# Optimization experiments

Hardware: AMD Instinct MI355X
Metric: run time of the kernel (lower is better)

The kernel has to match this reference:

```python
import jax, jax.numpy as jnp
import numpy as np

EPS = 1e-06
SIGMA_C = 2.0


def setup_inputs() -> dict:
    key = jax.random.key(0)
    k1, k2 = jax.random.split(key)
    B, L, D, T = 16, 512, 256, 2048
    text = jax.random.normal(k1, (B, L, D), dtype=jnp.float32)
    durs = jax.random.randint(k2, (B, L), 0, 8, dtype=jnp.int64)
    return {"text": text, "durs": durs, "total_time": T}


def reference(text, durs, total_time):
    # text: [B, L, D], durs: [B, L] int, total_time: static python int T
    d = durs.astype(jnp.float32)
    # NOTE: faithful to original: mean = durs/2 + cumsum(durs) (cumsum includes current dur)
    mean = d / 2.0 + jnp.cumsum(d, axis=-1)            # [B, L]
    sigma = d / SIGMA_C + EPS                          # [B, L]
    t = jnp.arange(total_time, dtype=jnp.float32) + 0.5  # [T]
    # Normal pdf evaluated at t: exp(log_prob) = exp(-0.5 z^2) / (sigma * sqrt(2 pi))
    z = (t[None, :, None] - mean[:, None, :]) / sigma[:, None, :]  # [B, T, L]
    inv_norm = 1.0 / (sigma[:, None, :] * jnp.sqrt(2.0 * jnp.pi))
    probs = jnp.exp(-0.5 * z * z) * inv_norm           # [B, T, L]
    probs = probs / (probs.sum(-1, keepdims=True) + EPS)
    return jnp.einsum("btl,bld->btd", probs, text)     # [B, T, D]
```

## Files before the change

### kernel.cpp

```cpp
#include <hip/hip_runtime.h>
#include <math.h>

#define L 512
#define TILE_T 16
#define NTHREADS 256
#define NACT_MAX 160
#define ZWIN 14.5f
#define NXCD 8

static constexpr float EPS = 1e-6f;
static constexpr float INV_SQRT_2PI = 0.39894228040143267794f;

__global__ __launch_bounds__(NTHREADS, 8) void ge_kernel(
    const float* __restrict__ text,
    const int*   __restrict__ durs,
    float*       __restrict__ out,
    int B, int D, int T, int tilesPerB, int nwg)
{
    __shared__ float s_lmean[NACT_MAX];
    __shared__ float s_lisig[NACT_MAX];
    __shared__ int   s_lrow[NACT_MAX];
    __shared__ float s_probs[NACT_MAX][TILE_T];
    __shared__ float s_wtot[4];
    __shared__ int   s_wcnt[4];
    __shared__ float s_wsum[4][TILE_T];
    __shared__ float s_norm[TILE_T];

    const int tid  = threadIdx.x;
    const int lane = tid & 63;
    const int wid  = tid >> 6;

    const int orig = blockIdx.x;
    const int wg   = (orig & (NXCD - 1)) * (nwg / NXCD) + (orig >> 3);
    const int b    = wg / tilesPerB;
    const int t0   = (wg % tilesPerB) * TILE_T;

    const int l0 = 2 * tid;
    const float d0 = (float)durs[b * L + l0];
    const float d1 = (float)durs[b * L + l0 + 1];
    const float pairsum = d0 + d1;

    float v = pairsum;
    #pragma unroll
    for (int off = 1; off < 64; off <<= 1) {
        float n = __shfl_up(v, off, 64);
        if (lane >= off) v += n;
    }
    if (lane == 63) s_wtot[wid] = v;
    __syncthreads();
    float wpre = 0.f;
    for (int w = 0; w < wid; ++w) wpre += s_wtot[w];
    const float excl = wpre + v - pairsum;

    const float cum0  = excl + d0;
    const float cum1  = cum0 + d1;
    const float mean0 = cum0 + 0.5f * d0;
    const float mean1 = cum1 + 0.5f * d1;
    const float sig0  = 0.5f * d0 + EPS;
    const float sig1  = 0.5f * d1 + EPS;
    const float isig0 = 1.0f / sig0;
    const float isig1 = 1.0f / sig1;

    const float tlo = (float)t0 + 0.5f;
    const float thi = (float)t0 + (float)TILE_T - 0.5f;
    const float r0 = ZWIN * sig0;
    const float r1 = ZWIN * sig1;
    const bool act0 = (d0 >= 1.f) && (mean0 + r0 >= tlo) && (mean0 - r0 <= thi);
    const bool act1 = (d1 >= 1.f) && (mean1 + r1 >= tlo) && (mean1 - r1 <= thi);

    const unsigned long long m0 = __ballot(act0);
    const unsigned long long m1 = __ballot(act1);
    const unsigned long long lt = (lane == 0) ? 0ull : ((~0ull) >> (64 - lane));
    const int off_in_wave = __popcll(m0 & lt) + __popcll(m1 & lt);
    const int cnt_wave = __popcll(m0) + __popcll(m1);
    if (lane == 0) s_wcnt[wid] = cnt_wave;
    __syncthreads();
    int base_w = 0;
    for (int w = 0; w < wid; ++w) base_w += s_wcnt[w];
    const int nact = s_wcnt[0] + s_wcnt[1] + s_wcnt[2] + s_wcnt[3];

    if (act0) {
        const int i = base_w + off_in_wave;
        s_lrow[i] = l0; s_lmean[i] = mean0; s_lisig[i] = isig0;
    }
    if (act1) {
        const int i = base_w + off_in_wave + (act0 ? 1 : 0);
        s_lrow[i] = l0 + 1; s_lmean[i] = mean1; s_lisig[i] = isig1;
    }
    __syncthreads();

    float psum = 0.f;
    const int   mytt = tid & 15;
    const float myt  = (float)(t0 + mytt) + 0.5f;
    const int total = nact * TILE_T;
    for (int idx = tid; idx < total; idx += NTHREADS) {
        const int i = idx >> 4;
        const float isg = s_lisig[i];
        const float z = (myt - s_lmean[i]) * isg;
        const float p = __expf(-0.5f * z * z) * isg * INV_SQRT_2PI;
        s_probs[i][mytt] = p;
        psum += p;
    }
    psum += __shfl_xor(psum, 16, 64);
    psum += __shfl_xor(psum, 32, 64);
    if (lane < 16) s_wsum[wid][lane] = psum;
    __syncthreads();
    if (tid < TILE_T) {
        const float s = s_wsum[0][tid] + s_wsum[1][tid] + s_wsum[2][tid] + s_wsum[3][tid];
        s_norm[tid] = 1.0f / (s + EPS);
    }
    __syncthreads();

    float4 a0 = {0,0,0,0}, a1 = {0,0,0,0}, a2 = {0,0,0,0}, a3 = {0,0,0,0};
    const float* tbase = text + (size_t)b * L * D + (lane << 2);
    if (nact > 0) {
        float4 vnext = *(const float4*)(tbase + (size_t)s_lrow[0] * D);
        for (int i = 0; i < nact; ++i) {
            const float4 val = vnext;
            if (i + 1 < nact)
                vnext = *(const float4*)(tbase + (size_t)s_lrow[i + 1] * D);
            const float4 p = *(const float4*)&s_probs[i][wid << 2];
            a0.x += p.x * val.x; a0.y += p.x * val.y; a0.z += p.x * val.z; a0.w += p.x * val.w;
            a1.x += p.y * val.x; a1.y += p.y * val.y; a1.z += p.y * val.z; a1.w += p.y * val.w;
            a2.x += p.z * val.x; a2.y += p.z * val.y; a2.z += p.z * val.z; a2.w += p.z * val.w;
            a3.x += p.w * val.x; a3.y += p.w * val.y; a3.z += p.w * val.z; a3.w += p.w * val.w;
        }
    }

    const float4 nrm = *(const float4*)&s_norm[wid << 2];
    const int tt0 = t0 + (wid << 2);
    float* obase = out + ((size_t)b * T + tt0) * D + (lane << 2);
    { float4 o = {a0.x*nrm.x, a0.y*nrm.x, a0.z*nrm.x, a0.w*nrm.x}; *(float4*)(obase + 0*(size_t)D) = o; }
    { float4 o = {a1.x*nrm.y, a1.y*nrm.y, a1.z*nrm.y, a1.w*nrm.y}; *(float4*)(obase + 1*(size_t)D) = o; }
    { float4 o = {a2.x*nrm.z, a2.y*nrm.z, a2.z*nrm.z, a2.w*nrm.z}; *(float4*)(obase + 2*(size_t)D) = o; }
    { float4 o = {a3.x*nrm.w, a3.y*nrm.w, a3.z*nrm.w, a3.w*nrm.w}; *(float4*)(obase + 3*(size_t)D) = o; }
}

extern "C" void kernel_launch(void* const* d_in, const int* in_sizes, int n_in,
                              void* d_out, int out_size, void* d_ws, size_t ws_size,
                              hipStream_t stream) {
    const float* text = (const float*)d_in[0];
    const int*   durs = (const int*)d_in[1];
    float*       out  = (float*)d_out;

    const int BL = in_sizes[1];
    const int D  = in_sizes[0] / BL;
    const int B  = BL / L;
    const int T  = out_size / (B * D);
    const int tilesPerB = (T + TILE_T - 1) / TILE_T;
    const int nwg = B * tilesPerB;

    ge_kernel<<<dim3(nwg), dim3(NTHREADS), 0, stream>>>(
        text, durs, out, B, D, T, tilesPerB, nwg);
}
```

Measured before the change: 18.09 us.

## Make each wave independently compute scan, active list, probs and norms without block barriers

Each wave now redundantly computes the full prefix sum over durations using int4 loads and an intra-wave scan. It then builds its own compacted active list for its 4 time steps and computes probabilities and normalisers with wave shuffles, which removes all __syncthreads. The Gaussian window shrinks from 14.5 to 9 sigma, the list is padded so the text-row gather loop can be unrolled by two, and bounds checks are added on the stores. The trade-off is redundant scan work per wave and a narrower truncation window, which may change numerics slightly.

New measurement: 19.05 us. 1.05x slower.

```diff
diff --git a/kernel.cpp b/kernel.cpp
--- a/kernel.cpp
+++ b/kernel.cpp
@@ -4,8 +4,9 @@
 #define L 512
 #define TILE_T 16
 #define NTHREADS 256
-#define NACT_MAX 160
-#define ZWIN 14.5f
+#define NWAVES 4
+#define NACT_PAD 104
+#define ZWIN 9.0f
 #define NXCD 8
 
 static constexpr float EPS = 1e-6f;
@@ -17,14 +18,9 @@
     float*       __restrict__ out,
     int B, int D, int T, int tilesPerB, int nwg)
 {
-    __shared__ float s_lmean[NACT_MAX];
-    __shared__ float s_lisig[NACT_MAX];
-    __shared__ int   s_lrow[NACT_MAX];
-    __shared__ float s_probs[NACT_MAX][TILE_T];
-    __shared__ float s_wtot[4];
-    __shared__ int   s_wcnt[4];
-    __shared__ float s_wsum[4][TILE_T];
-    __shared__ float s_norm[TILE_T];
+    __shared__ float2 s_mi [NWAVES][NACT_PAD];
+    __shared__ int    s_row[NWAVES][NACT_PAD];
+    __shared__ float  s_p  [NWAVES][4][NACT_PAD];
 
     const int tid  = threadIdx.x;
     const int lane = tid & 63;
@@ -35,105 +31,130 @@
     const int b    = wg / tilesPerB;
     const int t0   = (wg % tilesPerB) * TILE_T;
 
-    const int l0 = 2 * tid;
-    const float d0 = (float)durs[b * L + l0];
-    const float d1 = (float)durs[b * L + l0 + 1];
-    const float pairsum = d0 + d1;
-
-    float v = pairsum;
-    #pragma unroll
-    for (int off = 1; off < 64; off <<= 1) {
-        float n = __shfl_up(v, off, 64);
-        if (lane >= off) v += n;
+    const int r0 = lane << 3;
+    const int4* dp = (const int4*)(durs + (size_t)b * L + r0);
+    const int4 da = dp[0];
+    const int4 db = dp[1];
+    int dv[8] = {da.x, da.y, da.z, da.w, db.x, db.y, db.z, db.w};
+    int csum[8];
+    {
+        int run = 0;
+        #pragma unroll
+        for (int j = 0; j < 8; ++j) { run += dv[j]; csum[j] = run; }
+        int v = run;
+        #pragma unroll
+        for (int off = 1; off < 64; off <<= 1) {
+            int n = __shfl_up(v, off, 64);
+            if (lane >= off) v += n;
+        }
+        const int excl = v - run;
+        #pragma unroll
+        for (int j = 0; j < 8; ++j) csum[j] += excl;
     }
-    if (lane == 63) s_wtot[wid] = v;
-    __syncthreads();
-    float wpre = 0.f;
-    for (int w = 0; w < wid; ++w) wpre += s_wtot[w];
-    const float excl = wpre + v - pairsum;
-
-    const float cum0  = excl + d0;
-    const float cum1  = cum0 + d1;
-    const float mean0 = cum0 + 0.5f * d0;
-    const float mean1 = cum1 + 0.5f * d1;
-    const float sig0  = 0.5f * d0 + EPS;
-    const float sig1  = 0.5f * d1 + EPS;
-    const float isig0 = 1.0f / sig0;
-    const float isig1 = 1.0f / sig1;
 
     const float tlo = (float)t0 + 0.5f;
     const float thi = (float)t0 + (float)TILE_T - 0.5f;
-    const float r0 = ZWIN * sig0;
-    const float r1 = ZWIN * sig1;
-    const bool act0 = (d0 >= 1.f) && (mean0 + r0 >= tlo) && (mean0 - r0 <= thi);
-    const bool act1 = (d1 >= 1.f) && (mean1 + r1 >= tlo) && (mean1 - r1 <= thi);
 
-    const unsigned long long m0 = __ballot(act0);
-    const unsigned long long m1 = __ballot(act1);
-    const unsigned long long lt = (lane == 0) ? 0ull : ((~0ull) >> (64 - lane));
-    const int off_in_wave = __popcll(m0 & lt) + __popcll(m1 & lt);
-    const int cnt_wave = __popcll(m0) + __popcll(m1);
-    if (lane == 0) s_wcnt[wid] = cnt_wave;
-    __syncthreads();
-    int base_w = 0;
-    for (int w = 0; w < wid; ++w) base_w += s_wcnt[w];
-    const int nact = s_wcnt[0] + s_wcnt[1] + s_wcnt[2] + s_wcnt[3];
+    float meanv[8], isigv[8];
+    bool  act[8];
+    #pragma unroll
+    for (int j = 0; j < 8; ++j) {
+        const float d  = (float)dv[j];
+        const float m  = (float)csum[j] + 0.5f * d;
+        const float sg = 0.5f * d + EPS;
+        meanv[j] = m;
+        isigv[j] = 1.0f / sg;
+        const float r = ZWIN * sg;
+        act[j] = (dv[j] >= 1) && (m + r >= tlo) && (m - r <= thi);
+    }
+    const unsigned long long ltm = (lane == 0) ? 0ull : ((~0ull) >> (64 - lane));
+    int nact = 0;
+    #pragma unroll
+    for (int j = 0; j < 8; ++j) {
+        const unsigned long long mj = __ballot(act[j]);
+        if (act[j]) {
+            const int idx = nact + (int)__popcll(mj & ltm);
+            s_mi [wid][idx] = make_float2(meanv[j], isigv[j]);
+            s_row[wid][idx] = r0 + j;
+        }
+        nact += (int)__popcll(mj);
+    }
+    if (lane < 4) {
+        s_row[wid][nact + lane]  = 0;
+        s_p[wid][0][nact + lane] = 0.f;
+        s_p[wid][1][nact + lane] = 0.f;
+        s_p[wid][2][nact + lane] = 0.f;
+        s_p[wid][3][nact + lane] = 0.f;
+    }
+    asm volatile("s_waitcnt lgkmcnt(0)" ::: "memory");
+    __builtin_amdgcn_sched_barrier(0);
 
-    if (act0) {
-        const int i = base_w + off_in_wave;
-        s_lrow[i] = l0; s_lmean[i] = mean0; s_lisig[i] = isig0;
+    const float tq = (float)(t0 + (wid << 2)) + 0.5f;
+    float ps0 = 0.f, ps1 = 0.f, ps2 = 0.f, ps3 = 0.f;
+    for (int base_i = 0; base_i < nact; base_i += 64) {
+        const int item = base_i + lane;
+        if (item < nact) {
+            const float2 mi = s_mi[wid][item];
+            const float c  = mi.y * INV_SQRT_2PI;
+            const float z0 = (tq + 0.f - mi.x) * mi.y;
+            const float z1 = (tq + 1.f - mi.x) * mi.y;
+            const float z2 = (tq + 2.f - mi.x) * mi.y;
+            const float z3 = (tq + 3.f - mi.x) * mi.y;
+            const float p0 = __expf(-0.5f * z0 * z0) * c;
+            const float p1 = __expf(-0.5f * z1 * z1) * c;
+            const float p2 = __expf(-0.5f * z2 * z2) * c;
+            const float p3 = __expf(-0.5f * z3 * z3) * c;
+            s_p[wid][0][item] = p0;
+            s_p[wid][1][item] = p1;
+            s_p[wid][2][item] = p2;
+            s_p[wid][3][item] = p3;
+            ps0 += p0; ps1 += p1; ps2 += p2; ps3 += p3;
+        }
     }
-    if (act1) {
-        const int i = base_w + off_in_wave + (act0 ? 1 : 0);
-        s_lrow[i] = l0 + 1; s_lmean[i] = mean1; s_lisig[i] = isig1;
+    #pragma unroll
+    for (int off = 32; off > 0; off >>= 1) {
+        ps0 += __shfl_xor(ps0, off, 64);
+        ps1 += __shfl_xor(ps1, off, 64);
+        ps2 += __shfl_xor(ps2, off, 64);
+        ps3 += __shfl_xor(ps3, off, 64);
     }
-    __syncthreads();
-
-    float psum = 0.f;
-    const int   mytt = tid & 15;
-    const float myt  = (float)(t0 + mytt) + 0.5f;
-    const int total = nact * TILE_T;
-    for (int idx = tid; idx < total; idx += NTHREADS) {
-        const int i = idx >> 4;
-        const float isg = s_lisig[i];
-        const float z = (myt - s_lmean[i]) * isg;
-        const float p = __expf(-0.5f * z * z) * isg * INV_SQRT_2PI;
-        s_probs[i][mytt] = p;
-        psum += p;
-    }
-    psum += __shfl_xor(psum, 16, 64);
-    psum += __shfl_xor(psum, 32, 64);
-    if (lane < 16) s_wsum[wid][lane] = psum;
-    __syncthreads();
-    if (tid < TILE_T) {
-        const float s = s_wsum[0][tid] + s_wsum[1][tid] + s_wsum[2][tid] + s_wsum[3][tid];
-        s_norm[tid] = 1.0f / (s + EPS);
-    }
-    __syncthreads();
+    const float rn0 = 1.0f / (ps0 + EPS);
+    const float rn1 = 1.0f / (ps1 + EPS);
+    const float rn2 = 1.0f / (ps2 + EPS);
+    const float rn3 = 1.0f / (ps3 + EPS);
+    asm volatile("s_waitcnt lgkmcnt(0)" ::: "memory");
+    __builtin_amdgcn_sched_barrier(0);
 
     float4 a0 = {0,0,0,0}, a1 = {0,0,0,0}, a2 = {0,0,0,0}, a3 = {0,0,0,0};
-    const float* tbase = text + (size_t)b * L * D + (lane << 2);
+    const float* tb = text + (size_t)b * L * D + (lane << 2);
     if (nact > 0) {
-        float4 vnext = *(const float4*)(tbase + (size_t)s_lrow[0] * D);
-        for (int i = 0; i < nact; ++i) {
-            const float4 val = vnext;
-            if (i + 1 < nact)
-                vnext = *(const float4*)(tbase + (size_t)s_lrow[i + 1] * D);
-            const float4 p = *(const float4*)&s_probs[i][wid << 2];
-            a0.x += p.x * val.x; a0.y += p.x * val.y; a0.z += p.x * val.z; a0.w += p.x * val.w;
-            a1.x += p.y * val.x; a1.y += p.y * val.y; a1.z += p.y * val.z; a1.w += p.y * val.w;
-            a2.x += p.z * val.x; a2.y += p.z * val.y; a2.z += p.z * val.z; a2.w += p.z * val.w;
-            a3.x += p.w * val.x; a3.y += p.w * val.y; a3.z += p.w * val.z; a3.w += p.w * val.w;
+        float4 v0 = *(const float4*)(tb + (size_t)s_row[wid][0] * D);
+        float4 v1 = *(const float4*)(tb + (size_t)s_row[wid][1] * D);
+        const int niter = (nact + 1) & ~1;
+        for (int i = 0; i < niter; i += 2) {
+            const float4 w0 = v0;
+            const float4 w1 = v1;
+            v0 = *(const float4*)(tb + (size_t)s_row[wid][i + 2] * D);
+            v1 = *(const float4*)(tb + (size_t)s_row[wid][i + 3] * D);
+            const float q00 = s_p[wid][0][i],     q10 = s_p[wid][1][i],     q20 = s_p[wid][2][i],     q30 = s_p[wid][3][i];
+            const float q01 = s_p[wid][0][i + 1], q11 = s_p[wid][1][i + 1], q21 = s_p[wid][2][i + 1], q31 = s_p[wid][3][i + 1];
+            a0.x += q00*w0.x; a0.y += q00*w0.y; a0.z += q00*w0.z; a0.w += q00*w0.w;
+            a1.x += q10*w0.x; a1.y += q10*w0.y; a1.z += q10*w0.z; a1.w += q10*w0.w;
+            a2.x += q20*w0.x; a2.y += q20*w0.y; a2.z += q20*w0.z; a2.w += q20*w0.w;
+            a3.x += q30*w0.x; a3.y += q30*w0.y; a3.z += q30*w0.z; a3.w += q30*w0.w;
+            a0.x += q01*w1.x; a0.y += q01*w1.y; a0.z += q01*w1.z; a0.w += q01*w1.w;
+            a1.x += q11*w1.x; a1.y += q11*w1.y; a1.z += q11*w1.z; a1.w += q11*w1.w;
+            a2.x += q21*w1.x; a2.y += q21*w1.y; a2.z += q21*w1.z; a2.w += q21*w1.w;
+            a3.x += q31*w1.x; a3.y += q31*w1.y; a3.z += q31*w1.z; a3.w += q31*w1.w;
         }
     }
 
-    const float4 nrm = *(const float4*)&s_norm[wid << 2];
-    const int tt0 = t0 + (wid << 2);
-    float* obase = out + ((size_t)b * T + tt0) * D + (lane << 2);
-    { float4 o = {a0.x*nrm.x, a0.y*nrm.x, a0.z*nrm.x, a0.w*nrm.x}; *(float4*)(obase + 0*(size_t)D) = o; }
-    { float4 o = {a1.x*nrm.y, a1.y*nrm.y, a1.z*nrm.y, a1.w*nrm.y}; *(float4*)(obase + 1*(size_t)D) = o; }
-    { float4 o = {a2.x*nrm.z, a2.y*nrm.z, a2.z*nrm.z, a2.w*nrm.z}; *(float4*)(obase + 2*(size_t)D) = o; }
-    { float4 o = {a3.x*nrm.w, a3.y*nrm.w, a3.z*nrm.w, a3.w*nrm.w}; *(float4*)(obase + 3*(size_t)D) = o; }
+    const int ttq = t0 + (wid << 2);
+    float* ob = out + ((size_t)b * T + ttq) * D + (lane << 2);
+    if (ttq + 0 < T) *(float4*)(ob + 0*(size_t)D) = make_float4(a0.x*rn0, a0.y*rn0, a0.z*rn0, a0.w*rn0);
+    if (ttq + 1 < T) *(float4*)(ob + 1*(size_t)D) = make_float4(a1.x*rn1, a1.y*rn1, a1.z*rn1, a1.w*rn1);
+    if (ttq + 2 < T) *(float4*)(ob + 2*(size_t)D) = make_float4(a2.x*rn2, a2.y*rn2, a2.z*rn2, a2.w*rn2);
+    if (ttq + 3 < T) *(float4*)(ob + 3*(size_t)D) = make_float4(a3.x*rn3, a3.y*rn3, a3.z*rn3, a3.w*rn3);
 }
 
 extern "C" void kernel_launch(void* const* d_in, const int* in_sizes, int n_in,
```

## Use bf16 MFMA with pre-transposed text and contiguous active window

Applied to the files above, without the earlier changes.

Adds a prep kernel that transposes text to a padded bf16 [B,D,L] workspace, then a main kernel that computes the Gaussian weights in registers as bf16 A fragments and accumulates with 16x16x32 bf16 MFMA over a contiguous range of active L indices. It narrows the z-window and drops the LDS probs staging, compaction and several block barriers. The intent is to replace scalar FP32 FMA loops and gather-style text loads with matrix-core work. In exchange it adds an extra launch plus a full text read/write each call, and bf16 rounding of weights and text, which lowers accuracy. The old kernel stays as a fallback when D differs or the workspace is too small.

New measurement: 21.32 us. +17.9%, slower.

```diff
diff --git a/kernel.cpp b/kernel.cpp
--- a/kernel.cpp
+++ b/kernel.cpp
@@ -4,18 +4,160 @@
 #define L 512
 #define TILE_T 16
 #define NTHREADS 256
-#define NACT_MAX 160
-#define ZWIN 14.5f
+#define ZWIN 9.0f
 #define NXCD 8
+#define LPAD 544
+
+typedef __attribute__((ext_vector_type(8))) short bf16x8;
+typedef __attribute__((ext_vector_type(4))) float f32x4;
 
 static constexpr float EPS = 1e-6f;
 static constexpr float INV_SQRT_2PI = 0.39894228040143267794f;
 
-__global__ __launch_bounds__(NTHREADS, 8) void ge_kernel(
-    const float* __restrict__ text,
-    const int*   __restrict__ durs,
-    float*       __restrict__ out,
-    int B, int D, int T, int tilesPerB, int nwg)
+__device__ __forceinline__ unsigned int rne_bf16(float f) {
+    const unsigned int u = __float_as_uint(f);
+    return (u + 0x7fffu + ((u >> 16) & 1u)) >> 16;
+}
+
+__global__ __launch_bounds__(NTHREADS) void ge_prep(
+    const float* __restrict__ text, unsigned short* __restrict__ tT)
+{
+    const int tid = threadIdx.x;
+    const int b   = blockIdx.x >> 4;
+    const int l0  = (blockIdx.x & 15) << 5;
+    const float* src = text + ((size_t)b * L + l0) * 256 + tid;
+    unsigned int pk[16];
+    #pragma unroll
+    for (int j = 0; j < 16; ++j) {
+        const float f0 = src[(size_t)(2 * j) * 256];
+        const float f1 = src[(size_t)(2 * j + 1) * 256];
+        pk[j] = rne_bf16(f0) | (rne_bf16(f1) << 16);
+    }
+    uint4* dst = (uint4*)(tT + ((size_t)b * 256 + tid) * LPAD + l0);
+    dst[0] = make_uint4(pk[0],  pk[1],  pk[2],  pk[3]);
+    dst[1] = make_uint4(pk[4],  pk[5],  pk[6],  pk[7]);
+    dst[2] = make_uint4(pk[8],  pk[9],  pk[10], pk[11]);
+    dst[3] = make_uint4(pk[12], pk[13], pk[14], pk[15]);
+}
+
+__global__ __launch_bounds__(NTHREADS, 6) void ge_mfma(
+    const int*            __restrict__ durs,
+    const unsigned short* __restrict__ tT,
+    float*                __restrict__ out,
+    int B, int T, int tilesPerB, int nwg)
+{
+    __shared__ float2 s_mi[L];
+    __shared__ float  s_rn[TILE_T];
+
+    const int tid  = threadIdx.x;
+    const int lane = tid & 63;
+    const int wid  = tid >> 6;
+    const int g    = lane >> 4;
+    const int mrow = lane & 15;
+
+    const int orig = blockIdx.x;
+    const int wg   = (nwg % NXCD == 0) ? (orig & (NXCD - 1)) * (nwg / NXCD) + (orig >> 3)
+                                       : orig;
+    const int b    = wg / tilesPerB;
+    const int t0   = (wg % tilesPerB) * TILE_T;
+
+    const int r0 = lane << 3;
+    const int4 da = ((const int4*)(durs + (size_t)b * L + r0))[0];
+    const int4 db = ((const int4*)(durs + (size_t)b * L + r0))[1];
+    int dv[8] = {da.x, da.y, da.z, da.w, db.x, db.y, db.z, db.w};
+    int cs[8];
+    int run = 0;
+    #pragma unroll
+    for (int j = 0; j < 8; ++j) { run += dv[j]; cs[j] = run; }
+    int v = run;
+    #pragma unroll
+    for (int off = 1; off < 64; off <<= 1) {
+        int n = __shfl_up(v, off, 64);
+        if (lane >= off) v += n;
+    }
+    const int excl = v - run;
+
+    const float tlo = (float)t0 + 0.5f, thi = (float)t0 + 15.5f;
+    int mn = L, mx = -1;
+    #pragma unroll
+    for (int j = 0; j < 8; ++j) {
+        const float d  = (float)dv[j];
+        const float m  = (float)(cs[j] + excl) + 0.5f * d;
+        const float sg = 0.5f * d + EPS;
+        s_mi[r0 + j] = make_float2(m, 1.0f / sg);
+        const float r = ZWIN * sg;
+        if (dv[j] >= 1 && m + r >= tlo && m - r <= thi) {
+            mn = min(mn, r0 + j);
+            mx = max(mx, r0 + j);
+        }
+    }
+    #pragma unroll
+    for (int off = 32; off > 0; off >>= 1) {
+        mn = min(mn, __shfl_xor(mn, off, 64));
+        mx = max(mx, __shfl_xor(mx, off, 64));
+    }
+    asm volatile("s_waitcnt lgkmcnt(0)" ::: "memory");
+    __builtin_amdgcn_sched_barrier(0);
+
+    f32x4 acc0 = {0,0,0,0}, acc1 = {0,0,0,0}, acc2 = {0,0,0,0}, acc3 = {0,0,0,0};
+    float psum = 0.f;
+    const float tf = (float)(t0 + mrow) + 0.5f;
+    const unsigned short* tb = tT + ((size_t)b * 256 + (wid << 6) + mrow) * LPAD;
+
+    for (int kb = (mn & ~7); kb <= mx; kb += 32) {
+        const int k0 = kb + (g << 3);
+        bf16x8 af;
+        #pragma unroll
+        for (int j = 0; j < 8; ++j) {
+            const int k = k0 + j;
+            const float2 mi = s_mi[k & (L - 1)];
+            const float u = (tf - mi.x) * mi.y;
+            float p = __expf(-0.5f * u * u) * mi.y * INV_SQRT_2PI;
+            p = (k <= mx) ? p : 0.f;
+            const unsigned int h = rne_bf16(p);
+            psum += __uint_as_float(h << 16);
+            af[j] = (short)h;
+        }
+        const bf16x8 bf0 = *(const bf16x8*)(tb + (size_t)0 * 16 * LPAD + k0);
+        const bf16x8 bf1 = *(const bf16x8*)(tb + (size_t)1 * 16 * LPAD + k0);
+        const bf16x8 bf2 = *(const bf16x8*)(tb + (size_t)2 * 16 * LPAD + k0);
+        const bf16x8 bf3 = *(const bf16x8*)(tb + (size_t)3 * 16 * LPAD + k0);
+        acc0 = __builtin_amdgcn_mfma_f32_16x16x32_bf16(af, bf0, acc0, 0, 0, 0);
+        acc1 = __builtin_amdgcn_mfma_f32_16x16x32_bf16(af, bf1, acc1, 0, 0, 0);
+        acc2 = __builtin_amdgcn_mfma_f32_16x16x32_bf16(af, bf2, acc2, 0, 0, 0);
+        acc3 = __builtin_amdgcn_mfma_f32_16x16x32_bf16(af, bf3, acc3, 0, 0, 0);
+    }
+
+    psum += __shfl_xor(psum, 16, 64);
+    psum += __shfl_xor(psum, 32, 64);
+    const float rn = 1.0f / (psum + EPS);
+    if (lane < 16) s_rn[lane] = rn;
+    asm volatile("s_waitcnt lgkmcnt(0)" ::: "memory");
+    __builtin_amdgcn_sched_barrier(0);
+
+    const int trow = g << 2;
+    const float rr0 = s_rn[trow + 0];
+    const float rr1 = s_rn[trow + 1];
+    const float rr2 = s_rn[trow + 2];
+    const float rr3 = s_rn[trow + 3];
+    float* ob = out + ((size_t)b * T + t0 + trow) * 256 + (wid << 6) + mrow;
+    if (t0 + trow + 3 < T) {
+        ob[0*256 +  0] = acc0[0] * rr0;  ob[1*256 +  0] = acc0[1] * rr1;
+        ob[2*256 +  0] = acc0[2] * rr2;  ob[3*256 +  0] = acc0[3] * rr3;
+        ob[0*256 + 16] = acc1[0] * rr0;  ob[1*256 + 16] = acc1[1] * rr1;
+        ob[2*256 + 16] = acc1[2] * rr2;  ob[3*256 + 16] = acc1[3] * rr3;
+        ob[0*256 + 32] = acc2[0] * rr0;  ob[1*256 + 32] = acc2[1] * rr1;
+        ob[2*256 + 32] = acc2[2] * rr2;  ob[3*256 + 32] = acc2[3] * rr3;
+        ob[0*256 + 48] = acc3[0] * rr0;  ob[1*256 + 48] = acc3[1] * rr1;
+        ob[2*256 + 48] = acc3[2] * rr2;  ob[3*256 + 48] = acc3[3] * rr3;
+    }
+}
+
+#define NACT_MAX 160
+#define ZWINF 14.5f
+__global__ __launch_bounds__(NTHREADS, 8) void ge_fb(
+    const float* __restrict__ text, const int* __restrict__ durs,
+    float* __restrict__ out, int B, int D, int T, int tilesPerB, int nwg)
 {
     __shared__ float s_lmean[NACT_MAX];
     __shared__ float s_lisig[NACT_MAX];
@@ -25,75 +167,43 @@
     __shared__ int   s_wcnt[4];
     __shared__ float s_wsum[4][TILE_T];
     __shared__ float s_norm[TILE_T];
-
-    const int tid  = threadIdx.x;
-    const int lane = tid & 63;
-    const int wid  = tid >> 6;
-
+    const int tid = threadIdx.x, lane = tid & 63, wid = tid >> 6;
     const int orig = blockIdx.x;
-    const int wg   = (orig & (NXCD - 1)) * (nwg / NXCD) + (orig >> 3);
-    const int b    = wg / tilesPerB;
-    const int t0   = (wg % tilesPerB) * TILE_T;
-
+    const int wg = (orig & (NXCD - 1)) * (nwg / NXCD) + (orig >> 3);
+    const int b = wg / tilesPerB, t0 = (wg % tilesPerB) * TILE_T;
     const int l0 = 2 * tid;
-    const float d0 = (float)durs[b * L + l0];
-    const float d1 = (float)durs[b * L + l0 + 1];
+    const float d0 = (float)durs[b * L + l0], d1 = (float)durs[b * L + l0 + 1];
     const float pairsum = d0 + d1;
-
     float v = pairsum;
     #pragma unroll
-    for (int off = 1; off < 64; off <<= 1) {
-        float n = __shfl_up(v, off, 64);
-        if (lane >= off) v += n;
-    }
+    for (int off = 1; off < 64; off <<= 1) { float n = __shfl_up(v, off, 64); if (lane >= off) v += n; }
     if (lane == 63) s_wtot[wid] = v;
     __syncthreads();
     float wpre = 0.f;
     for (int w = 0; w < wid; ++w) wpre += s_wtot[w];
     const float excl = wpre + v - pairsum;
-
-    const float cum0  = excl + d0;
-    const float cum1  = cum0 + d1;
-    const float mean0 = cum0 + 0.5f * d0;
-    const float mean1 = cum1 + 0.5f * d1;
-    const float sig0  = 0.5f * d0 + EPS;
-    const float sig1  = 0.5f * d1 + EPS;
-    const float isig0 = 1.0f / sig0;
-    const float isig1 = 1.0f / sig1;
-
-    const float tlo = (float)t0 + 0.5f;
-    const float thi = (float)t0 + (float)TILE_T - 0.5f;
-    const float r0 = ZWIN * sig0;
-    const float r1 = ZWIN * sig1;
-    const bool act0 = (d0 >= 1.f) && (mean0 + r0 >= tlo) && (mean0 - r0 <= thi);
-    const bool act1 = (d1 >= 1.f) && (mean1 + r1 >= tlo) && (mean1 - r1 <= thi);
-
-    const unsigned long long m0 = __ballot(act0);
-    const unsigned long long m1 = __ballot(act1);
+    const float cum0 = excl + d0, cum1 = cum0 + d1;
+    const float mean0 = cum0 + 0.5f * d0, mean1 = cum1 + 0.5f * d1;
+    const float sig0 = 0.5f * d0 + EPS, sig1 = 0.5f * d1 + EPS;
+    const float isig0 = 1.0f / sig0, isig1 = 1.0f / sig1;
+    const float tlo = (float)t0 + 0.5f, thi = (float)t0 + 15.5f;
+    const bool act0 = (d0 >= 1.f) && (mean0 + ZWINF * sig0 >= tlo) && (mean0 - ZWINF * sig0 <= thi);
+    const bool act1 = (d1 >= 1.f) && (mean1 + ZWINF * sig1 >= tlo) && (mean1 - ZWINF * sig1 <= thi);
+    const unsigned long long m0 = __ballot(act0), m1 = __ballot(act1);
     const unsigned long long lt = (lane == 0) ? 0ull : ((~0ull) >> (64 - lane));
-    const int off_in_wave = __popcll(m0 & lt) + __popcll(m1 & lt);
-    const int cnt_wave = __popcll(m0) + __popcll(m1);
-    if (lane == 0) s_wcnt[wid] = cnt_wave;
+    const int offw = __popcll(m0 & lt) + __popcll(m1 & lt);
+    if (lane == 0) s_wcnt[wid] = __popcll(m0) + __popcll(m1);
     __syncthreads();
     int base_w = 0;
     for (int w = 0; w < wid; ++w) base_w += s_wcnt[w];
     const int nact = s_wcnt[0] + s_wcnt[1] + s_wcnt[2] + s_wcnt[3];
-
-    if (act0) {
-        const int i = base_w + off_in_wave;
-        s_lrow[i] = l0; s_lmean[i] = mean0; s_lisig[i] = isig0;
-    }
-    if (act1) {
-        const int i = base_w + off_in_wave + (act0 ? 1 : 0);
-        s_lrow[i] = l0 + 1; s_lmean[i] = mean1; s_lisig[i] = isig1;
-    }
-    __syncthreads();
-
+    if (act0) { const int i = base_w + offw; s_lrow[i] = l0; s_lmean[i] = mean0; s_lisig[i] = isig0; }
+    if (act1) { const int i = base_w + offw + (act0 ? 1 : 0); s_lrow[i] = l0 + 1; s_lmean[i] = mean1; s_lisig[i] = isig1; }
+    __syncthreads();
     float psum = 0.f;
-    const int   mytt = tid & 15;
-    const float myt  = (float)(t0 + mytt) + 0.5f;
-    const int total = nact * TILE_T;
-    for (int idx = tid; idx < total; idx += NTHREADS) {
+    const int mytt = tid & 15;
+    const float myt = (float)(t0 + mytt) + 0.5f;
+    for (int idx = tid; idx < nact * TILE_T; idx += NTHREADS) {
         const int i = idx >> 4;
         const float isg = s_lisig[i];
         const float z = (myt - s_lmean[i]) * isg;
@@ -110,23 +220,20 @@
         s_norm[tid] = 1.0f / (s + EPS);
     }
     __syncthreads();
-
     float4 a0 = {0,0,0,0}, a1 = {0,0,0,0}, a2 = {0,0,0,0}, a3 = {0,0,0,0};
     const float* tbase = text + (size_t)b * L * D + (lane << 2);
     if (nact > 0) {
         float4 vnext = *(const float4*)(tbase + (size_t)s_lrow[0] * D);
         for (int i = 0; i < nact; ++i) {
             const float4 val = vnext;
-            if (i + 1 < nact)
-                vnext = *(const float4*)(tbase + (size_t)s_lrow[i + 1] * D);
+            if (i + 1 < nact) vnext = *(const float4*)(tbase + (size_t)s_lrow[i + 1] * D);
             const float4 p = *(const float4*)&s_probs[i][wid << 2];
-            a0.x += p.x * val.x; a0.y += p.x * val.y; a0.z += p.x * val.z; a0.w += p.x * val.w;
-            a1.x += p.y * val.x; a1.y += p.y * val.y; a1.z += p.y * val.z; a1.w += p.y * val.w;
-            a2.x += p.z * val.x; a2.y += p.z * val.y; a2.z += p.z * val.z; a2.w += p.z * val.w;
-            a3.x += p.w * val.x; a3.y += p.w * val.y; a3.z += p.w * val.z; a3.w += p.w * val.w;
+            a0.x += p.x*val.x; a0.y += p.x*val.y; a0.z += p.x*val.z; a0.w += p.x*val.w;
+            a1.x += p.y*val.x; a1.y += p.y*val.y; a1.z += p.y*val.z; a1.w += p.y*val.w;
+            a2.x += p.z*val.x; a2.y += p.z*val.y; a2.z += p.z*val.z; a2.w += p.z*val.w;
+            a3.x += p.w*val.x; a3.y += p.w*val.y; a3.z += p.w*val.z; a3.w += p.w*val.w;
         }
     }
-
     const float4 nrm = *(const float4*)&s_norm[wid << 2];
     const int tt0 = t0 + (wid << 2);
     float* obase = out + ((size_t)b * T + tt0) * D + (lane << 2);
@@ -150,6 +257,12 @@
     const int tilesPerB = (T + TILE_T - 1) / TILE_T;
     const int nwg = B * tilesPerB;
 
-    ge_kernel<<<dim3(nwg), dim3(NTHREADS), 0, stream>>>(
-        text, durs, out, B, D, T, tilesPerB, nwg);
-}
+    const size_t needT = (size_t)B * 256 * LPAD * sizeof(unsigned short);
+    if (D == 256 && ws_size >= needT) {
+        unsigned short* tT = (unsigned short*)d_ws;
+        ge_prep<<<dim3(B * 16), dim3(NTHREADS), 0, stream>>>(text, tT);
+        ge_mfma<<<dim3(nwg),    dim3(NTHREADS), 0, stream>>>(durs, tT, out, B, T, tilesPerB, nwg);
+    } else {
+        ge_fb<<<dim3(nwg), dim3(NTHREADS), 0, stream>>>(text, durs, out, B, D, T, tilesPerB, nwg);
+    }
+}
```
